# Performance work log

Measured on AMD Instinct MI355X. Metric: run time of the kernel, lower is better.

The kernel has to match this reference:

```python
import jax, jax.numpy as jnp
import numpy as np

B, T, DH, DS, A = 32, 2048, 1024, 1024, 512

def setup_inputs() -> dict:
    key = jax.random.key(0)
    k1, k2, k3, k4, k5 = jax.random.split(key, 5)
    s = jax.random.normal(k1, (B, DS), dtype=jnp.float32)
    h = jax.random.normal(k2, (B, T, DH), dtype=jnp.float32)
    # glorot_uniform for W_a, U_a; uniform(-0.05, 0.05) for v_a (Keras defaults)
    lim_W = np.sqrt(6.0 / (DS + A)).astype(np.float32)
    lim_U = np.sqrt(6.0 / (DH + A)).astype(np.float32)
    W_a = jax.random.uniform(k3, (DS, A), minval=-lim_W, maxval=lim_W, dtype=jnp.float32)
    U_a = jax.random.uniform(k4, (DH, A), minval=-lim_U, maxval=lim_U, dtype=jnp.float32)
    v_a = jax.random.uniform(k5, (A,), minval=-0.05, maxval=0.05, dtype=jnp.float32)
    return {"s": s, "h": h, "W_a": W_a, "U_a": U_a, "v_a": v_a}

def reference(s, h, W_a, U_a, v_a):
    # U_a_h: [B, T, A]; W_a_s: [B, 1, A]
    U_a_h = jnp.einsum('btd,da->bta', h, U_a)
    W_a_s = (s @ W_a)[:, None, :]
    e = jnp.tanh(W_a_s + U_a_h)          # [B, T, A]
    e = jnp.einsum('bta,a->bt', e, v_a)   # learned-vector reduction
    a = jax.nn.softmax(e, axis=-1)        # exp / sum over time (same math, stable)
    c = jnp.einsum('bt,btd->bd', a, h)    # weighted sum over time
    return c
```

## Files before the change

kernel.cpp:

```cpp
#include <hip/hip_runtime.h>
#include <hip/hip_bf16.h>

#define B_  32
#define T_  2048
#define DH_ 1024
#define DS_ 1024
#define A_  512
#define M_  (B_ * T_)

typedef __attribute__((ext_vector_type(8))) short bf16x8;
typedef __attribute__((ext_vector_type(4))) float f32x4;

__device__ __forceinline__ unsigned short f2bf(float f) {
    union { float f; unsigned u; } v; v.f = f;
    unsigned r = 0x7FFFu + ((v.u >> 16) & 1u);
    return (unsigned short)((v.u + r) >> 16);
}
__device__ __forceinline__ float fast_tanh(float x) {
    float cx = fminf(fmaxf(x, -9.f), 9.f);
    float e2 = __expf(2.f * cx);
    return (e2 - 1.f) / (e2 + 1.f);
}
__device__ __forceinline__ unsigned pack_bf2(float lo, float hi) {
    union { float f; unsigned u; } a, b;
    a.f = lo; b.f = hi;
    return __builtin_amdgcn_perm(b.u + 0x8000u, a.u + 0x8000u, 0x07060302u);
}

__global__ void zero_e(float* __restrict__ e) {
    e[blockIdx.x * 256 + threadIdx.x] = 0.f;
}

__global__ void prep_ut(const float* __restrict__ U, unsigned short* __restrict__ Ut) {
    int o = blockIdx.x * 256 + threadIdx.x;
    int a = o >> 10, k = o & (DH_ - 1);
    Ut[o] = f2bf(U[k * A_ + a]);
}

__global__ void ws_gemv2(const float* __restrict__ s, const float* __restrict__ W,
                         float* __restrict__ Ws) {
    __shared__ float red[4][64];
    const int blk = blockIdx.x;
    const int b = blk >> 3, a0 = (blk & 7) * 64;
    const int tid = threadIdx.x;
    const int a = a0 + (tid & 63), kq = tid >> 6;
    const float* sp = s + b * DS_ + kq * 256;
    const float* wp = W + (size_t)(kq * 256) * A_ + a;
    float acc = 0.f;
#pragma unroll 8
    for (int k = 0; k < 256; ++k) acc += sp[k] * wp[(size_t)k * A_];
    red[kq][tid & 63] = acc;
    __syncthreads();
    if (tid < 64)
        Ws[b * A_ + a0 + tid] = red[0][tid] + red[1][tid] + red[2][tid] + red[3][tid];
}

__global__ void __launch_bounds__(256, 4)
gemm_e3(const float* __restrict__ h,
        const unsigned short* __restrict__ Ut,
        const float* __restrict__ Ws, const float* __restrict__ va,
        float* __restrict__ e) {
    __shared__ unsigned short As[2][128][40];
    __shared__ unsigned short Bs[2][128][32];

    const int tid = threadIdx.x;
    const int bid0 = blockIdx.x;
    const int bid = (bid0 & 7) * 256 + (bid0 >> 3);
    const int tn = bid & 3, tm = bid >> 2;
    const int rowBase = tm * 128, nBase = tn * 128;

    const int lane = tid & 63;
    const int wid = tid >> 6;
    const int wm = wid >> 1, wn = wid & 1;
    const int lr = lane & 15, kg = lane >> 4;

    const int aRow = tid >> 3;
    const int aColF = (tid & 7) * 4;

    f32x4 acc[4][4];
#pragma unroll
    for (int i = 0; i < 4; ++i)
#pragma unroll
        for (int j = 0; j < 4; ++j) acc[i][j] = (f32x4){0.f, 0.f, 0.f, 0.f};

    auto stageB = [&](int buf, int kt) {
        const int k0 = kt * 32;
#pragma unroll
        for (int q = 0; q < 2; ++q) {
            int b = q * 4096 + tid * 16;
            int r = b >> 6;
            int col = (b & 63) >> 1;
            const unsigned short* gb = Ut + (size_t)(nBase + r) * DH_ + k0 + col;
            __builtin_amdgcn_global_load_lds(
                (const __attribute__((address_space(1))) unsigned int*)gb,
                (__attribute__((address_space(3))) unsigned int*)(&Bs[buf][0][0] + (b >> 1)),
                16, 0, 0);
        }
    };

    auto loadA = [&](float4* areg, int kt) {
        const int k0 = kt * 32;
#pragma unroll
        for (int j = 0; j < 4; ++j) {
            int row = j * 32 + aRow;
            areg[j] = *(const float4*)(h + (size_t)(rowBase + row) * DH_ + k0 + aColF);
        }
    };

    auto writeA = [&](const float4* areg, int buf) {
#pragma unroll
        for (int j = 0; j < 4; ++j) {
            int row = j * 32 + aRow;
            uint2 u;
            u.x = pack_bf2(areg[j].x, areg[j].y);
            u.y = pack_bf2(areg[j].z, areg[j].w);
            *(uint2*)(&As[buf][row][aColF]) = u;
        }
    };

    float4 areg[4];
    stageB(0, 0);
    loadA(areg, 0);
    writeA(areg, 0);
    __syncthreads();

#pragma unroll 1
    for (int kt = 0; kt < DH_ / 32; ++kt) {
        const int buf = kt & 1;
        const bool more = (kt < DH_ / 32 - 1);
        if (more) {
            stageB(buf ^ 1, kt + 1);
            loadA(areg, kt + 1);
        }

        bf16x8 af[4], bq[4];
#pragma unroll
        for (int mi = 0; mi < 4; ++mi)
            af[mi] = *(const bf16x8*)(&As[buf][wm * 64 + mi * 16 + lr][kg * 8]);
#pragma unroll
        for (int nf = 0; nf < 4; ++nf)
            bq[nf] = *(const bf16x8*)(&Bs[buf][wn * 64 + nf * 16 + lr][kg * 8]);
#pragma unroll
        for (int mi = 0; mi < 4; ++mi)
#pragma unroll
            for (int nf = 0; nf < 4; ++nf)
                acc[mi][nf] = __builtin_amdgcn_mfma_f32_16x16x32_bf16(
                    af[mi], bq[nf], acc[mi][nf], 0, 0, 0);

        if (more) writeA(areg, buf ^ 1);
        __syncthreads();
    }

    const int bIdx = rowBase >> 11;
    const float* WsRow = Ws + bIdx * A_;
    float wsv[4], vav[4];
#pragma unroll
    for (int nf = 0; nf < 4; ++nf) {
        int a = nBase + wn * 64 + nf * 16 + lr;
        wsv[nf] = WsRow[a];
        vav[nf] = va[a];
    }
#pragma unroll
    for (int mi = 0; mi < 4; ++mi) {
#pragma unroll
        for (int j = 0; j < 4; ++j) {
            float ssum = 0.f;
#pragma unroll
            for (int nf = 0; nf < 4; ++nf) {
                float x = acc[mi][nf][j] + wsv[nf];
                ssum += fast_tanh(x) * vav[nf];
            }
            ssum += __shfl_xor(ssum, 1);
            ssum += __shfl_xor(ssum, 2);
            ssum += __shfl_xor(ssum, 4);
            ssum += __shfl_xor(ssum, 8);
            if (lr == 0) {
                int row = rowBase + wm * 64 + mi * 16 + kg * 4 + j;
                atomicAdd(&e[row], ssum);
            }
        }
    }
}

__global__ void smax_ctx(const float* __restrict__ e, const float* __restrict__ h,
                         float* __restrict__ c) {
    __shared__ float al[T_];
    __shared__ float red[8];
    __shared__ float part[256];
    const int b = blockIdx.x >> 3, dseg = blockIdx.x & 7;
    const int tid = threadIdx.x;
    const float* ep = e + (size_t)b * T_;

    float4 v0 = ((const float4*)ep)[tid * 2];
    float4 v1 = ((const float4*)ep)[tid * 2 + 1];
    float m = fmaxf(fmaxf(fmaxf(v0.x, v0.y), fmaxf(v0.z, v0.w)),
                    fmaxf(fmaxf(v1.x, v1.y), fmaxf(v1.z, v1.w)));
#pragma unroll
    for (int off = 1; off < 64; off <<= 1) m = fmaxf(m, __shfl_xor(m, off));
    const int wv = tid >> 6;
    if ((tid & 63) == 0) red[wv] = m;
    __syncthreads();
    m = fmaxf(fmaxf(red[0], red[1]), fmaxf(red[2], red[3]));
    float e0 = __expf(v0.x - m), e1 = __expf(v0.y - m);
    float e2 = __expf(v0.z - m), e3 = __expf(v0.w - m);
    float e4 = __expf(v1.x - m), e5 = __expf(v1.y - m);
    float e6 = __expf(v1.z - m), e7 = __expf(v1.w - m);
    float ssum = e0 + e1 + e2 + e3 + e4 + e5 + e6 + e7;
#pragma unroll
    for (int off = 1; off < 64; off <<= 1) ssum += __shfl_xor(ssum, off);
    if ((tid & 63) == 0) red[4 + wv] = ssum;
    al[tid * 8 + 0] = e0; al[tid * 8 + 1] = e1;
    al[tid * 8 + 2] = e2; al[tid * 8 + 3] = e3;
    al[tid * 8 + 4] = e4; al[tid * 8 + 5] = e5;
    al[tid * 8 + 6] = e6; al[tid * 8 + 7] = e7;
    __syncthreads();
    const float inv = 1.f / (red[4] + red[5] + red[6] + red[7]);

    const int d = dseg * 128 + (tid & 127);
    const int th = tid >> 7;
    const float* hp = h + ((size_t)b * T_ + th) * DH_ + d;
    float acc = 0.f;
#pragma unroll 8
    for (int t = 0; t < T_ / 2; ++t)
        acc += al[2 * t + th] * hp[(size_t)(2 * t) * DH_];
    part[tid] = acc;
    __syncthreads();
    if (tid < 128)
        c[(size_t)b * DH_ + dseg * 128 + tid] = (part[tid] + part[tid + 128]) * inv;
}

extern "C" void kernel_launch(void* const* d_in, const int* in_sizes, int n_in,
                              void* d_out, int out_size, void* d_ws, size_t ws_size,
                              hipStream_t stream) {
    const float* s   = (const float*)d_in[0];
    const float* h   = (const float*)d_in[1];
    const float* W_a = (const float*)d_in[2];
    const float* U_a = (const float*)d_in[3];
    const float* v_a = (const float*)d_in[4];
    float* c = (float*)d_out;

    float* e  = (float*)d_ws;
    float* Ws = e + M_;
    unsigned short* Ut = (unsigned short*)(Ws + B_ * A_);

    zero_e<<<M_ / 256, 256, 0, stream>>>(e);
    prep_ut<<<(A_ * DH_) / 256, 256, 0, stream>>>(U_a, Ut);
    ws_gemv2<<<B_ * 8, 256, 0, stream>>>(s, W_a, Ws);
    gemm_e3<<<(M_ / 128) * (A_ / 128), 256, 0, stream>>>(h, Ut, Ws, v_a, e);
    smax_ctx<<<B_ * 8, 256, 0, stream>>>(e, h, c);
}
```

Before: 199.7 us.

## Pre-convert h to bf16 and pipeline GEMM with triple-buffered direct LDS loads

Adds a pass that converts h once to bf16 in workspace. The attention-score GEMM then streams both operands straight into LDS with global_load_lds, using 256x128 tiles, 512 threads, XOR-swizzled LDS, a three-stage buffer with vmcnt-based waits and raised priority around the MFMAs. The context kernel reads the bf16 copy of h instead of fp32, halving its bytes. This aims to cut the repeated fp32 reads of h and the register round-trip for in-kernel conversion. In exchange it adds a full conversion pass, a larger workspace, and bf16 rounding in the context sum.

Result: slower. 235.3 us (+17.9%).

```diff
diff --git a/kernel.cpp b/kernel.cpp
--- a/kernel.cpp
+++ b/kernel.cpp
@@ -16,6 +16,12 @@
     unsigned r = 0x7FFFu + ((v.u >> 16) & 1u);
     return (unsigned short)((v.u + r) >> 16);
 }
+__device__ __forceinline__ float bflo(unsigned u) {
+    union { unsigned u; float f; } v; v.u = u << 16; return v.f;
+}
+__device__ __forceinline__ float bfhi(unsigned u) {
+    union { unsigned u; float f; } v; v.u = u & 0xFFFF0000u; return v.f;
+}
 __device__ __forceinline__ float fast_tanh(float x) {
     float cx = fminf(fmaxf(x, -9.f), 9.f);
     float e2 = __expf(2.f * cx);
@@ -35,6 +41,18 @@
     int o = blockIdx.x * 256 + threadIdx.x;
     int a = o >> 10, k = o & (DH_ - 1);
     Ut[o] = f2bf(U[k * A_ + a]);
+}
+
+__global__ void conv_h(const float* __restrict__ h, unsigned int* __restrict__ hb) {
+    size_t i = ((size_t)blockIdx.x * 256 + threadIdx.x) * 8;
+    float4 a = *(const float4*)(h + i);
+    float4 b = *(const float4*)(h + i + 4);
+    uint4 o;
+    o.x = pack_bf2(a.x, a.y);
+    o.y = pack_bf2(a.z, a.w);
+    o.z = pack_bf2(b.x, b.y);
+    o.w = pack_bf2(b.z, b.w);
+    *(uint4*)(hb + i / 2) = o;
 }
 
 __global__ void ws_gemv2(const float* __restrict__ s, const float* __restrict__ W,
@@ -55,27 +73,25 @@
         Ws[b * A_ + a0 + tid] = red[0][tid] + red[1][tid] + red[2][tid] + red[3][tid];
 }
 
-__global__ void __launch_bounds__(256, 4)
-gemm_e3(const float* __restrict__ h,
-        const unsigned short* __restrict__ Ut,
-        const float* __restrict__ Ws, const float* __restrict__ va,
-        float* __restrict__ e) {
-    __shared__ unsigned short As[2][128][40];
-    __shared__ unsigned short Bs[2][128][32];
+__global__ void __launch_bounds__(512, 1)
+gemm_pipe(const unsigned short* __restrict__ hb,
+          const unsigned short* __restrict__ Ut,
+          const float* __restrict__ Ws, const float* __restrict__ va,
+          float* __restrict__ e) {
+    __shared__ unsigned short As[3][256][64];
+    __shared__ unsigned short Bs[3][128][64];
 
     const int tid = threadIdx.x;
     const int bid0 = blockIdx.x;
-    const int bid = (bid0 & 7) * 256 + (bid0 >> 3);
+    const int bid = (bid0 & 7) * 128 + (bid0 >> 3);
     const int tn = bid & 3, tm = bid >> 2;
-    const int rowBase = tm * 128, nBase = tn * 128;
+    const int rowBase = tm * 256, nBase = tn * 128;
 
     const int lane = tid & 63;
     const int wid = tid >> 6;
     const int wm = wid >> 1, wn = wid & 1;
     const int lr = lane & 15, kg = lane >> 4;
-
-    const int aRow = tid >> 3;
-    const int aColF = (tid & 7) * 4;
+    const int x7 = lane & 7;
 
     f32x4 acc[4][4];
 #pragma unroll
@@ -83,73 +99,81 @@
 #pragma unroll
         for (int j = 0; j < 4; ++j) acc[i][j] = (f32x4){0.f, 0.f, 0.f, 0.f};
 
-    auto stageB = [&](int buf, int kt) {
-        const int k0 = kt * 32;
-#pragma unroll
-        for (int q = 0; q < 2; ++q) {
-            int b = q * 4096 + tid * 16;
-            int r = b >> 6;
-            int col = (b & 63) >> 1;
-            const unsigned short* gb = Ut + (size_t)(nBase + r) * DH_ + k0 + col;
+    auto stageA = [&](int buf, int tile) {
+        const int k0 = tile * 64;
+#pragma unroll
+        for (int j = 0; j < 4; ++j) {
+            int byt = j * 8192 + tid * 16;
+            int r = byt >> 7;
+            int g = ((byt >> 4) & 7) ^ (r & 7);
+            const unsigned short* ga = hb + (size_t)(rowBase + r) * DH_ + k0 + g * 8;
+            __builtin_amdgcn_global_load_lds(
+                (const __attribute__((address_space(1))) unsigned int*)ga,
+                (__attribute__((address_space(3))) unsigned int*)(&As[buf][0][0] + (byt >> 1)),
+                16, 0, 0);
+        }
+    };
+    auto stageB = [&](int buf, int tile) {
+        const int k0 = tile * 64;
+#pragma unroll
+        for (int j = 0; j < 2; ++j) {
+            int byt = j * 8192 + tid * 16;
+            int r = byt >> 7;
+            int g = ((byt >> 4) & 7) ^ (r & 7);
+            const unsigned short* gb = Ut + (size_t)(nBase + r) * DH_ + k0 + g * 8;
             __builtin_amdgcn_global_load_lds(
                 (const __attribute__((address_space(1))) unsigned int*)gb,
-                (__attribute__((address_space(3))) unsigned int*)(&Bs[buf][0][0] + (b >> 1)),
+                (__attribute__((address_space(3))) unsigned int*)(&Bs[buf][0][0] + (byt >> 1)),
                 16, 0, 0);
         }
     };
 
-    auto loadA = [&](float4* areg, int kt) {
-        const int k0 = kt * 32;
-#pragma unroll
-        for (int j = 0; j < 4; ++j) {
-            int row = j * 32 + aRow;
-            areg[j] = *(const float4*)(h + (size_t)(rowBase + row) * DH_ + k0 + aColF);
-        }
-    };
-
-    auto writeA = [&](const float4* areg, int buf) {
-#pragma unroll
-        for (int j = 0; j < 4; ++j) {
-            int row = j * 32 + aRow;
-            uint2 u;
-            u.x = pack_bf2(areg[j].x, areg[j].y);
-            u.y = pack_bf2(areg[j].z, areg[j].w);
-            *(uint2*)(&As[buf][row][aColF]) = u;
-        }
-    };
-
-    float4 areg[4];
-    stageB(0, 0);
-    loadA(areg, 0);
-    writeA(areg, 0);
-    __syncthreads();
+    stageA(0, 0); stageB(0, 0);
+    stageA(1, 1); stageB(1, 1);
 
 #pragma unroll 1
-    for (int kt = 0; kt < DH_ / 32; ++kt) {
-        const int buf = kt & 1;
-        const bool more = (kt < DH_ / 32 - 1);
-        if (more) {
-            stageB(buf ^ 1, kt + 1);
-            loadA(areg, kt + 1);
-        }
-
-        bf16x8 af[4], bq[4];
-#pragma unroll
-        for (int mi = 0; mi < 4; ++mi)
-            af[mi] = *(const bf16x8*)(&As[buf][wm * 64 + mi * 16 + lr][kg * 8]);
-#pragma unroll
-        for (int nf = 0; nf < 4; ++nf)
-            bq[nf] = *(const bf16x8*)(&Bs[buf][wn * 64 + nf * 16 + lr][kg * 8]);
-#pragma unroll
-        for (int mi = 0; mi < 4; ++mi)
-#pragma unroll
-            for (int nf = 0; nf < 4; ++nf)
-                acc[mi][nf] = __builtin_amdgcn_mfma_f32_16x16x32_bf16(
-                    af[mi], bq[nf], acc[mi][nf], 0, 0, 0);
-
-        if (more) writeA(areg, buf ^ 1);
-        __syncthreads();
-    }
+    for (int t = 0; t < DH_ / 64; ++t) {
+        asm volatile("s_waitcnt vmcnt(6)" ::: "memory");
+        __builtin_amdgcn_s_barrier();
+        __builtin_amdgcn_sched_barrier(0);
+
+        const int buf = t % 3;
+        const unsigned short* Ab = &As[buf][0][0];
+        const unsigned short* Bb = &Bs[buf][0][0];
+
+        bf16x8 af[2][4], bq[2][4];
+#pragma unroll
+        for (int kh = 0; kh < 2; ++kh) {
+            const int gsw = ((kh * 4 + kg) ^ x7) * 8;
+#pragma unroll
+            for (int nf = 0; nf < 4; ++nf) {
+                int rb = wn * 64 + nf * 16 + lr;
+                bq[kh][nf] = *(const bf16x8*)(Bb + rb * 64 + gsw);
+            }
+#pragma unroll
+            for (int mf = 0; mf < 4; ++mf) {
+                int ra = wm * 64 + mf * 16 + lr;
+                af[kh][mf] = *(const bf16x8*)(Ab + ra * 64 + gsw);
+            }
+        }
+
+        const int tt = (t + 2) & 15;
+        const int buf2 = (t + 2) % 3;
+        stageA(buf2, tt);
+        stageB(buf2, tt);
+
+        __builtin_amdgcn_s_setprio(1);
+#pragma unroll
+        for (int kh = 0; kh < 2; ++kh)
+#pragma unroll
+            for (int mf = 0; mf < 4; ++mf)
+#pragma unroll
+                for (int nf = 0; nf < 4; ++nf)
+                    acc[mf][nf] = __builtin_amdgcn_mfma_f32_16x16x32_bf16(
+                        af[kh][mf], bq[kh][nf], acc[mf][nf], 0, 0, 0);
+        __builtin_amdgcn_s_setprio(0);
+    }
+    asm volatile("s_waitcnt vmcnt(0)" ::: "memory");
 
     const int bIdx = rowBase >> 11;
     const float* WsRow = Ws + bIdx * A_;
@@ -161,13 +185,13 @@
         vav[nf] = va[a];
     }
 #pragma unroll
-    for (int mi = 0; mi < 4; ++mi) {
+    for (int mf = 0; mf < 4; ++mf) {
 #pragma unroll
         for (int j = 0; j < 4; ++j) {
             float ssum = 0.f;
 #pragma unroll
             for (int nf = 0; nf < 4; ++nf) {
-                float x = acc[mi][nf][j] + wsv[nf];
+                float x = acc[mf][nf][j] + wsv[nf];
                 ssum += fast_tanh(x) * vav[nf];
             }
             ssum += __shfl_xor(ssum, 1);
@@ -175,18 +199,18 @@
             ssum += __shfl_xor(ssum, 4);
             ssum += __shfl_xor(ssum, 8);
             if (lr == 0) {
-                int row = rowBase + wm * 64 + mi * 16 + kg * 4 + j;
+                int row = rowBase + wm * 64 + mf * 16 + kg * 4 + j;
                 atomicAdd(&e[row], ssum);
             }
         }
     }
 }
 
-__global__ void smax_ctx(const float* __restrict__ e, const float* __restrict__ h,
+__global__ void smax_ctx(const float* __restrict__ e, const unsigned int* __restrict__ hb,
                          float* __restrict__ c) {
     __shared__ float al[T_];
     __shared__ float red[8];
-    __shared__ float part[256];
+    __shared__ float2 part[256];
     const int b = blockIdx.x >> 3, dseg = blockIdx.x & 7;
     const int tid = threadIdx.x;
     const float* ep = e + (size_t)b * T_;
@@ -216,17 +240,26 @@
     __syncthreads();
     const float inv = 1.f / (red[4] + red[5] + red[6] + red[7]);
 
-    const int d = dseg * 128 + (tid & 127);
-    const int th = tid >> 7;
-    const float* hp = h + ((size_t)b * T_ + th) * DH_ + d;
-    float acc = 0.f;
+    const int cu = dseg * 64 + (tid & 63);
+    const int ts = tid >> 6;
+    const unsigned int* hp = hb + ((size_t)b * T_ + ts) * (DH_ / 2) + cu;
+    float a0 = 0.f, a1 = 0.f;
 #pragma unroll 8
-    for (int t = 0; t < T_ / 2; ++t)
-        acc += al[2 * t + th] * hp[(size_t)(2 * t) * DH_];
-    part[tid] = acc;
-    __syncthreads();
-    if (tid < 128)
-        c[(size_t)b * DH_ + dseg * 128 + tid] = (part[tid] + part[tid + 128]) * inv;
+    for (int i = 0; i < T_ / 4; ++i) {
+        float w = al[4 * i + ts];
+        unsigned int v = hp[(size_t)(4 * i) * (DH_ / 2)];
+        a0 += w * bflo(v);
+        a1 += w * bfhi(v);
+    }
+    part[tid] = make_float2(a0, a1);
+    __syncthreads();
+    if (tid < 64) {
+        float2 p0 = part[tid], p1 = part[tid + 64], p2 = part[tid + 128], p3 = part[tid + 192];
+        float r0 = (p0.x + p1.x + p2.x + p3.x) * inv;
+        float r1 = (p0.y + p1.y + p2.y + p3.y) * inv;
+        float* cp = c + (size_t)b * DH_ + dseg * 128 + tid * 2;
+        cp[0] = r0; cp[1] = r1;
+    }
 }
 
 extern "C" void kernel_launch(void* const* d_in, const int* in_sizes, int n_in,
@@ -239,13 +272,19 @@
     const float* v_a = (const float*)d_in[4];
     float* c = (float*)d_out;
 
+    const size_t off_Ws = (size_t)M_ * 4;
+    const size_t off_Ut = off_Ws + (size_t)B_ * A_ * 4;
+    const size_t off_hb = off_Ut + (size_t)A_ * DH_ * 2;
+
     float* e  = (float*)d_ws;
-    float* Ws = e + M_;
-    unsigned short* Ut = (unsigned short*)(Ws + B_ * A_);
+    float* Ws = (float*)((char*)d_ws + off_Ws);
+    unsigned short* Ut = (unsigned short*)((char*)d_ws + off_Ut);
+    unsigned short* hb = (unsigned short*)((char*)d_ws + off_hb);
 
     zero_e<<<M_ / 256, 256, 0, stream>>>(e);
     prep_ut<<<(A_ * DH_) / 256, 256, 0, stream>>>(U_a, Ut);
     ws_gemv2<<<B_ * 8, 256, 0, stream>>>(s, W_a, Ws);
-    gemm_e3<<<(M_ / 128) * (A_ / 128), 256, 0, stream>>>(h, Ut, Ws, v_a, e);
-    smax_ctx<<<B_ * 8, 256, 0, stream>>>(e, h, c);
-}
+    conv_h<<<(M_ * (size_t)DH_) / (256 * 8), 256, 0, stream>>>(h, (unsigned int*)hb);
+    gemm_pipe<<<(M_ / 256) * (A_ / 128), 512, 0, stream>>>(hb, Ut, Ws, v_a, e);
+    smax_ctx<<<B_ * 8, 256, 0, stream>>>(e, (const unsigned int*)hb, c);
+}
```

## Restructure GEMM mainloop with K=64 tiles, triple-buffered B, XOR swizzle

Applied to the files above, without the earlier changes.

The GEMM mainloop now uses 64-wide K tiles and a three-stage buffer for B, loaded asynchronously through global_load_lds. A single barrier per iteration is gated by an explicit vmcnt wait. LDS layouts switch from padding to an XOR swizzle to avoid bank conflicts, and MFMA issue is wrapped in setprio to favour the math. The aim is to halve the barrier count, deepen prefetch, and hide load latency. In exchange, LDS use and register pressure rise and launch bounds drop to 2 blocks per SIMD, which risks lower occupancy.

Measured after the change: 265.3 us. +32.9%, slower.

```diff
diff --git a/kernel.cpp b/kernel.cpp
--- a/kernel.cpp
+++ b/kernel.cpp
@@ -55,13 +55,13 @@
         Ws[b * A_ + a0 + tid] = red[0][tid] + red[1][tid] + red[2][tid] + red[3][tid];
 }
 
-__global__ void __launch_bounds__(256, 4)
-gemm_e3(const float* __restrict__ h,
+__global__ void __launch_bounds__(256, 2)
+gemm_v3(const float* __restrict__ h,
         const unsigned short* __restrict__ Ut,
         const float* __restrict__ Ws, const float* __restrict__ va,
         float* __restrict__ e) {
-    __shared__ unsigned short As[2][128][40];
-    __shared__ unsigned short Bs[2][128][32];
+    __shared__ unsigned short As[2][128][64];
+    __shared__ unsigned short Bs[3][128][64];
 
     const int tid = threadIdx.x;
     const int bid0 = blockIdx.x;
@@ -74,8 +74,9 @@
     const int wm = wid >> 1, wn = wid & 1;
     const int lr = lane & 15, kg = lane >> 4;
 
-    const int aRow = tid >> 3;
-    const int aColF = (tid & 7) * 4;
+    const int ar = tid >> 1;
+    const int acf = (tid & 1) * 32;
+    const int agb = (tid & 1) * 4;
 
     f32x4 acc[4][4];
 #pragma unroll
@@ -83,72 +84,86 @@
 #pragma unroll
         for (int j = 0; j < 4; ++j) acc[i][j] = (f32x4){0.f, 0.f, 0.f, 0.f};
 
-    auto stageB = [&](int buf, int kt) {
-        const int k0 = kt * 32;
-#pragma unroll
-        for (int q = 0; q < 2; ++q) {
-            int b = q * 4096 + tid * 16;
-            int r = b >> 6;
-            int col = (b & 63) >> 1;
-            const unsigned short* gb = Ut + (size_t)(nBase + r) * DH_ + k0 + col;
+    auto stageB = [&](int buf, int tile) {
+        const int k0 = tile * 64;
+#pragma unroll
+        for (int j = 0; j < 4; ++j) {
+            int byt = j * 4096 + tid * 16;
+            int r = byt >> 7;
+            int g = ((byt >> 4) & 7) ^ (r & 7);
+            const unsigned short* gb = Ut + (size_t)(nBase + r) * DH_ + k0 + g * 8;
             __builtin_amdgcn_global_load_lds(
                 (const __attribute__((address_space(1))) unsigned int*)gb,
-                (__attribute__((address_space(3))) unsigned int*)(&Bs[buf][0][0] + (b >> 1)),
+                (__attribute__((address_space(3))) unsigned int*)(&Bs[buf][0][0] + (byt >> 1)),
                 16, 0, 0);
         }
     };
-
-    auto loadA = [&](float4* areg, int kt) {
-        const int k0 = kt * 32;
-#pragma unroll
-        for (int j = 0; j < 4; ++j) {
-            int row = j * 32 + aRow;
-            areg[j] = *(const float4*)(h + (size_t)(rowBase + row) * DH_ + k0 + aColF);
-        }
+    auto loadA = [&](float4* areg, int tile) {
+        const int k0 = tile * 64;
+        const float* hp = h + (size_t)(rowBase + ar) * DH_ + k0 + acf;
+#pragma unroll
+        for (int j = 0; j < 8; ++j) areg[j] = *(const float4*)(hp + j * 4);
     };
-
-    auto writeA = [&](const float4* areg, int buf) {
-#pragma unroll
-        for (int j = 0; j < 4; ++j) {
-            int row = j * 32 + aRow;
-            uint2 u;
-            u.x = pack_bf2(areg[j].x, areg[j].y);
-            u.y = pack_bf2(areg[j].z, areg[j].w);
-            *(uint2*)(&As[buf][row][aColF]) = u;
+    auto packwriteA = [&](const float4* areg, int buf) {
+#pragma unroll
+        for (int g4 = 0; g4 < 4; ++g4) {
+            uint4 u;
+            u.x = pack_bf2(areg[2 * g4].x, areg[2 * g4].y);
+            u.y = pack_bf2(areg[2 * g4].z, areg[2 * g4].w);
+            u.z = pack_bf2(areg[2 * g4 + 1].x, areg[2 * g4 + 1].y);
+            u.w = pack_bf2(areg[2 * g4 + 1].z, areg[2 * g4 + 1].w);
+            int gs = (agb + g4) ^ (ar & 7);
+            *(uint4*)(&As[buf][ar][gs * 8]) = u;
         }
     };
 
-    float4 areg[4];
+    float4 areg[8];
     stageB(0, 0);
+    stageB(1, 1);
     loadA(areg, 0);
-    writeA(areg, 0);
-    __syncthreads();
-
+    packwriteA(areg, 0);
+
+    const int NT = DH_ / 64;
 #pragma unroll 1
-    for (int kt = 0; kt < DH_ / 32; ++kt) {
-        const int buf = kt & 1;
-        const bool more = (kt < DH_ / 32 - 1);
-        if (more) {
-            stageB(buf ^ 1, kt + 1);
-            loadA(areg, kt + 1);
-        }
-
-        bf16x8 af[4], bq[4];
-#pragma unroll
-        for (int mi = 0; mi < 4; ++mi)
-            af[mi] = *(const bf16x8*)(&As[buf][wm * 64 + mi * 16 + lr][kg * 8]);
-#pragma unroll
-        for (int nf = 0; nf < 4; ++nf)
-            bq[nf] = *(const bf16x8*)(&Bs[buf][wn * 64 + nf * 16 + lr][kg * 8]);
-#pragma unroll
-        for (int mi = 0; mi < 4; ++mi)
-#pragma unroll
-            for (int nf = 0; nf < 4; ++nf)
-                acc[mi][nf] = __builtin_amdgcn_mfma_f32_16x16x32_bf16(
-                    af[mi], bq[nf], acc[mi][nf], 0, 0, 0);
-
-        if (more) writeA(areg, buf ^ 1);
-        __syncthreads();
+    for (int t = 0; t < NT; ++t) {
+        asm volatile("s_waitcnt vmcnt(4) lgkmcnt(0)" ::: "memory");
+        __builtin_amdgcn_s_barrier();
+        __builtin_amdgcn_sched_barrier(0);
+
+        if (t < NT - 2) stageB((t + 2) % 3, t + 2);
+        if (t < NT - 1) loadA(areg, t + 1);
+
+        const int abuf = t & 1;
+        const unsigned short* Ab = &As[abuf][0][0];
+        const unsigned short* Bb = &Bs[t % 3][0][0];
+
+        bf16x8 af[2][4], bq[2][4];
+#pragma unroll
+        for (int kh = 0; kh < 2; ++kh) {
+#pragma unroll
+            for (int nf = 0; nf < 4; ++nf) {
+                int rb = wn * 64 + nf * 16 + lr;
+                bq[kh][nf] = *(const bf16x8*)(Bb + rb * 64 + (((kh * 4 + kg) ^ (rb & 7)) * 8));
+            }
+#pragma unroll
+            for (int mf = 0; mf < 4; ++mf) {
+                int ra = wm * 64 + mf * 16 + lr;
+                af[kh][mf] = *(const bf16x8*)(Ab + ra * 64 + (((kh * 4 + kg) ^ (ra & 7)) * 8));
+            }
+        }
+
+        __builtin_amdgcn_s_setprio(1);
+#pragma unroll
+        for (int kh = 0; kh < 2; ++kh)
+#pragma unroll
+            for (int mf = 0; mf < 4; ++mf)
+#pragma unroll
+                for (int nf = 0; nf < 4; ++nf)
+                    acc[mf][nf] = __builtin_amdgcn_mfma_f32_16x16x32_bf16(
+                        af[kh][mf], bq[kh][nf], acc[mf][nf], 0, 0, 0);
+        __builtin_amdgcn_s_setprio(0);
+
+        if (t < NT - 1) packwriteA(areg, abuf ^ 1);
     }
 
     const int bIdx = rowBase >> 11;
@@ -161,13 +176,13 @@
         vav[nf] = va[a];
     }
 #pragma unroll
-    for (int mi = 0; mi < 4; ++mi) {
+    for (int mf = 0; mf < 4; ++mf) {
 #pragma unroll
         for (int j = 0; j < 4; ++j) {
             float ssum = 0.f;
 #pragma unroll
             for (int nf = 0; nf < 4; ++nf) {
-                float x = acc[mi][nf][j] + wsv[nf];
+                float x = acc[mf][nf][j] + wsv[nf];
                 ssum += fast_tanh(x) * vav[nf];
             }
             ssum += __shfl_xor(ssum, 1);
@@ -175,7 +190,7 @@
             ssum += __shfl_xor(ssum, 4);
             ssum += __shfl_xor(ssum, 8);
             if (lr == 0) {
-                int row = rowBase + wm * 64 + mi * 16 + kg * 4 + j;
+                int row = rowBase + wm * 64 + mf * 16 + kg * 4 + j;
                 atomicAdd(&e[row], ssum);
             }
         }
@@ -246,6 +261,6 @@
     zero_e<<<M_ / 256, 256, 0, stream>>>(e);
     prep_ut<<<(A_ * DH_) / 256, 256, 0, stream>>>(U_a, Ut);
     ws_gemv2<<<B_ * 8, 256, 0, stream>>>(s, W_a, Ws);
-    gemm_e3<<<(M_ / 128) * (A_ / 128), 256, 0, stream>>>(h, Ut, Ws, v_a, e);
+    gemm_v3<<<(M_ / 128) * (A_ / 128), 256, 0, stream>>>(h, Ut, Ws, v_a, e);
     smax_ctx<<<B_ * 8, 256, 0, stream>>>(e, h, c);
 }
```
